# Kernel tuning notes

Hardware: AMD Instinct MI355X
Metric: run time of the kernel (lower is better)

The kernel has to match this reference:

```python
import jax, jax.numpy as jnp
import numpy as np

NUM_HEADS = 12

def _get_rel_pos(size, rel_pos):
    # q_size == k_size == size, no interpolation needed (table has 2*size-1 rows)
    idx = jnp.arange(size)[:, None] - jnp.arange(size)[None, :] + (size - 1)  # (size,size)
    return rel_pos[idx]  # (size, size, head_dim)

def setup_inputs() -> dict:
    key = jax.random.key(0)
    ks = jax.random.split(key, 7)
    B, H, W, dim = 8, 32, 32, 768
    head_dim = dim // NUM_HEADS
    return {
        "x": jax.random.normal(ks[0], (B, H, W, dim), jnp.float32),
        "qkv_w": jax.random.normal(ks[1], (dim, 3 * dim), jnp.float32) * 0.02,
        "qkv_b": jax.random.normal(ks[2], (3 * dim,), jnp.float32) * 0.02,
        "proj_w": jax.random.normal(ks[3], (dim, dim), jnp.float32) * 0.02,
        "proj_b": jax.random.normal(ks[4], (dim,), jnp.float32) * 0.02,
        "rel_pos_h": jax.random.normal(ks[5], (2 * H - 1, head_dim), jnp.float32) * 0.02,
        "rel_pos_w": jax.random.normal(ks[6], (2 * W - 1, head_dim), jnp.float32) * 0.02,
    }

def reference(x, qkv_w, qkv_b, proj_w, proj_b, rel_pos_h, rel_pos_w):
    B, H, W, dim = x.shape
    N = H * W
    head_dim = dim // NUM_HEADS
    scale = head_dim ** (-0.5)

    qkv = x.reshape(B, N, dim) @ qkv_w + qkv_b                     # (B,N,3*dim)
    qkv = qkv.reshape(B, N, 3, NUM_HEADS, head_dim)
    qkv = qkv.transpose(2, 0, 3, 1, 4).reshape(3, B * NUM_HEADS, N, head_dim)
    q, k, v = qkv[0], qkv[1], qkv[2]                               # (B*h, N, hd)

    attn = jnp.einsum("bnd,bmd->bnm", q * scale, k)                # (B*h, N, N)

    # decomposed relative position bias
    Rh = _get_rel_pos(H, rel_pos_h)                                # (H,H,hd)
    Rw = _get_rel_pos(W, rel_pos_w)                                # (W,W,hd)
    r_q = q.reshape(B * NUM_HEADS, H, W, head_dim)
    rel_h = jnp.einsum("bhwc,hkc->bhwk", r_q, Rh)                  # (B*h,H,W,H)
    rel_w = jnp.einsum("bhwc,wkc->bhwk", r_q, Rw)                  # (B*h,H,W,W)
    attn = (attn.reshape(B * NUM_HEADS, H, W, H, W)
            + rel_h[:, :, :, :, None]
            + rel_w[:, :, :, None, :]).reshape(B * NUM_HEADS, N, N)

    attn = jax.nn.softmax(attn, axis=-1)
    out = jnp.einsum("bnm,bmd->bnd", attn, v)                      # (B*h, N, hd)
    out = out.reshape(B, NUM_HEADS, H, W, head_dim).transpose(0, 2, 3, 1, 4).reshape(B, H, W, dim)
    return out @ proj_w + proj_b
```

## Files before the change

kernel.cpp:

```cpp
#include <hip/hip_runtime.h>
#include <hip/hip_bf16.h>
#include <math.h>

#define DIM   768
#define NHEAD 12
#define NQ    1024

typedef short  short8  __attribute__((ext_vector_type(8)));
typedef unsigned short us8 __attribute__((ext_vector_type(8)));
typedef float  f32x16  __attribute__((ext_vector_type(16)));

#if __has_builtin(__builtin_amdgcn_exp2f)
#define EXP2(x) __builtin_amdgcn_exp2f(x)
#else
#define EXP2(x) __expf(0.69314718056f * (x))
#endif
#define LOG2E 1.44269504089f

__device__ inline ushort f2b(float f) {
  union { float f; unsigned u; } c; c.f = f;
  unsigned r = (c.u + 0x7FFFu + ((c.u >> 16) & 1u)) >> 16;
  return (ushort)r;
}
__device__ inline float b2f(ushort h) {
  union { unsigned u; float f; } c; c.u = ((unsigned)h) << 16;
  return c.f;
}
__device__ inline ushort4 cvt4(float4 v) {
  ushort4 o; o.x = f2b(v.x); o.y = f2b(v.y); o.z = f2b(v.z); o.w = f2b(v.w);
  return o;
}
__device__ inline unsigned pkr(float a, float b) {
  union { float f; unsigned u; } ca, cb; ca.f = a; cb.f = b;
  return __builtin_amdgcn_perm(cb.u + 0x8000u, ca.u + 0x8000u, 0x07060302u);
}

__global__ __launch_bounds__(256) void prep(
    const float* __restrict__ x, const float* __restrict__ qkv_w,
    const float* __restrict__ proj_w, ushort* __restrict__ Xb,
    ushort* __restrict__ Wqt, ushort* __restrict__ Wpt) {
  __shared__ ushort Ts[64][68];
  const int blk = blockIdx.x, tid = threadIdx.x;
  if (blk < 768) {
    const float4* src = (const float4*)x;
    ushort4* dst = (ushort4*)Xb;
    int base = blk * 2048;
#pragma unroll
    for (int it = 0; it < 8; ++it) {
      int i = base + it * 256 + tid;
      dst[i] = cvt4(src[i]);
    }
    return;
  }
  const float* W; ushort* Wt; int ncols, tk, tn;
  if (blk < 1200) { int t = blk - 768;  W = qkv_w; Wt = Wqt; ncols = 2304; tk = t % 12; tn = t / 12; }
  else            { int t = blk - 1200; W = proj_w; Wt = Wpt; ncols = 768; tk = t % 12; tn = t / 12; }
  const int kb = tk * 64, nb = tn * 64;
#pragma unroll
  for (int rr = 0; rr < 4; ++rr) {
    int r = (tid >> 4) + rr * 16, c4 = (tid & 15) * 4;
    float4 w = *(const float4*)(W + (size_t)(kb + r) * ncols + nb + c4);
    *(ushort4*)&Ts[r][c4] = cvt4(w);
  }
  __syncthreads();
#pragma unroll
  for (int wwi = 0; wwi < 2; ++wwi) {
    int n = (tid >> 3) + wwi * 32, k8 = (tid & 7) * 8;
    us8 v;
#pragma unroll
    for (int j = 0; j < 8; ++j) v[j] = Ts[k8 + j][n];
    *(us8*)(Wt + (size_t)(nb + n) * 768 + kb + k8) = v;
  }
}

template <int OUTBF>
__global__ __launch_bounds__(256, 3) void gemm_mfma(
    const ushort* __restrict__ A, const ushort* __restrict__ BT,
    const float* __restrict__ bias, void* __restrict__ Cp, int Nc,
    ushort* __restrict__ VTg) {
  __shared__ ushort Asl[128][72];
  __shared__ ushort Bsl[128][72];
  const int tid = threadIdx.x;
  const int bm = blockIdx.y * 128, bn = blockIdx.x * 128;
  const int lane = tid & 63, wv = tid >> 6;
  const int l31 = lane & 31, lh = lane >> 5;
  const int wm = (wv >> 1) * 64, wn = (wv & 1) * 64;

  f32x16 acc[2][2];
#pragma unroll
  for (int i = 0; i < 2; ++i)
#pragma unroll
    for (int j = 0; j < 2; ++j)
#pragma unroll
      for (int r = 0; r < 16; ++r) acc[i][j][r] = 0.f;

  for (int kt = 0; kt < 768; kt += 64) {
    __syncthreads();
#pragma unroll
    for (int it = 0; it < 4; ++it) {
      int item = tid + 256 * it;
      int r = item >> 3, c8 = (item & 7) * 8;
      *(us8*)&Asl[r][c8] = *(const us8*)(A + (size_t)(bm + r) * 768 + kt + c8);
      *(us8*)&Bsl[r][c8] = *(const us8*)(BT + (size_t)(bn + r) * 768 + kt + c8);
    }
    __syncthreads();
#pragma unroll
    for (int ks = 0; ks < 4; ++ks) {
      short8 a0 = *(const short8*)&Asl[wm + l31][ks * 16 + lh * 8];
      short8 a1 = *(const short8*)&Asl[wm + 32 + l31][ks * 16 + lh * 8];
      short8 b0 = *(const short8*)&Bsl[wn + l31][ks * 16 + lh * 8];
      short8 b1 = *(const short8*)&Bsl[wn + 32 + l31][ks * 16 + lh * 8];
      acc[0][0] = __builtin_amdgcn_mfma_f32_32x32x16_bf16(a0, b0, acc[0][0], 0, 0, 0);
      acc[0][1] = __builtin_amdgcn_mfma_f32_32x32x16_bf16(a0, b1, acc[0][1], 0, 0, 0);
      acc[1][0] = __builtin_amdgcn_mfma_f32_32x32x16_bf16(a1, b0, acc[1][0], 0, 0, 0);
      acc[1][1] = __builtin_amdgcn_mfma_f32_32x32x16_bf16(a1, b1, acc[1][1], 0, 0, 0);
    }
  }

  const bool vreg = OUTBF && (bn >= 1536);
  if (!vreg) {
#pragma unroll
    for (int mb = 0; mb < 2; ++mb)
#pragma unroll
      for (int nb = 0; nb < 2; ++nb) {
        int col = bn + wn + nb * 32 + l31;
        float bv = bias[col];
#pragma unroll
        for (int reg = 0; reg < 16; ++reg) {
          int row = bm + wm + mb * 32 + (reg & 3) + 8 * (reg >> 2) + 4 * lh;
          float o = acc[mb][nb][reg] + bv;
          if (OUTBF) ((ushort*)Cp)[(size_t)row * Nc + col] = f2b(o);
          else       ((float*)Cp)[(size_t)row * Nc + col] = o;
        }
      }
  } else {
    const int b_ = bm >> 10;
    const int nbase = (bm & 1023) + wm;
#pragma unroll
    for (int nb = 0; nb < 2; ++nb) {
      int col = bn + wn + nb * 32 + l31;
      float bv = bias[col];
      int hd_ = col - 1536;
      int h_ = hd_ >> 6, d_ = hd_ & 63;
      ushort* vrow = VTg + ((size_t)(b_ * NHEAD + h_) * 64 + d_) * NQ;
#pragma unroll
      for (int mb = 0; mb < 2; ++mb)
#pragma unroll
        for (int g = 0; g < 4; ++g) {
          int n = nbase + mb * 32 + 8 * g + 4 * lh;
          ushort4 st;
          st.x = f2b(acc[mb][nb][4 * g + 0] + bv);
          st.y = f2b(acc[mb][nb][4 * g + 1] + bv);
          st.z = f2b(acc[mb][nb][4 * g + 2] + bv);
          st.w = f2b(acc[mb][nb][4 * g + 3] + bv);
          *(ushort4*)(vrow + n) = st;
        }
    }
  }
}

__global__ __launch_bounds__(256) void bias_kernel(
    const ushort* __restrict__ QKV, const float* __restrict__ rph,
    const float* __restrict__ rpw, ushort* __restrict__ RH,
    ushort* __restrict__ RW) {
  __shared__ ushort Qb[128][72];
  __shared__ ushort Tb[63][72];

  const int tid = threadIdx.x;
  const int bh = blockIdx.x;
  const int gy = blockIdx.y;
  const int b = bh / NHEAD, h = bh % NHEAD;
  const bool isH = gy < 8;
  const int g4 = isH ? gy : (gy - 8);
  const int lane = tid & 63, wv = tid >> 6;
  const int l31 = lane & 31, lh = lane >> 5;

  const ushort* qb = QKV + (size_t)b * NQ * 2304 + h * 64;
  const float* tab = isH ? rph : rpw;

#pragma unroll
  for (int it = 0; it < 4; ++it) {
    int item = tid + 256 * it;
    if (item < 63 * 16) {
      int r = item >> 4, q4 = (item & 15) * 4;
      float4 v = *(const float4*)(tab + r * 64 + q4);
      *(ushort4*)&Tb[r][q4] = cvt4(v);
    }
  }
#pragma unroll
  for (int it = 0; it < 4; ++it) {
    int item = tid + 256 * it;
    int r = item >> 3, c8 = (item & 7) * 8;
    int n = isH ? (g4 * 128 + r) : ((r & 31) * 32 + g4 * 4 + (r >> 5));
    *(us8*)&Qb[r][c8] = *(const us8*)(qb + (size_t)n * 2304 + c8);
  }
  __syncthreads();

  const int fixed = g4 * 4 + wv;
  f32x16 acc;
#pragma unroll
  for (int i = 0; i < 16; ++i) acc[i] = 0.f;
#pragma unroll
  for (int ks = 0; ks < 4; ++ks) {
    short8 a  = *(const short8*)&Qb[wv * 32 + l31][ks * 16 + lh * 8];
    short8 bb = *(const short8*)&Tb[fixed + 31 - l31][ks * 16 + lh * 8];
    acc = __builtin_amdgcn_mfma_f32_32x32x16_bf16(a, bb, acc, 0, 0, 0);
  }
  ushort* outp = isH ? RH : RW;
#pragma unroll
  for (int reg = 0; reg < 16; ++reg) {
    int row = (reg & 3) + 8 * (reg >> 2) + 4 * lh;
    int n = isH ? (fixed * 32 + row) : (row * 32 + fixed);
    outp[((size_t)bh * NQ + n) * 32 + l31] = f2b(acc[reg] * LOG2E);
  }
}

__global__ __launch_bounds__(256, 3) void attn_mfma(
    const ushort* __restrict__ QKV, const ushort* __restrict__ VTg,
    const ushort* __restrict__ RH, const ushort* __restrict__ RW,
    ushort* __restrict__ O) {
  __shared__ ushort Qs[128][72];
  __shared__ ushort Ks[64][72];
  __shared__ ushort VT[64][72];

  const int tid = threadIdx.x;
  const int bh = blockIdx.x % 96;
  const int qt = blockIdx.x / 96;
  const int b = bh / NHEAD, h = bh % NHEAD;
  const int n0 = qt * 128;
  const int lane = tid & 63, wv = tid >> 6;
  const int l31 = lane & 31, lh = lane >> 5;
  const int wb = wv * 32;

  const ushort* qb = QKV + (size_t)b * NQ * 2304 + h * 64;
  const ushort* kb = qb + DIM;
  const ushort* vtg = VTg + (size_t)bh * 64 * NQ;

#pragma unroll
  for (int it = 0; it < 4; ++it) {
    int item = tid + 256 * it;
    int r = item >> 3, c8 = (item & 7) * 8;
    *(us8*)&Qs[r][c8] = *(const us8*)(qb + (size_t)(n0 + r) * 2304 + c8);
  }

  const int q = n0 + wb + l31;
  const ushort* rwrow = RW + ((size_t)bh * NQ + q) * 32;
  float rwv[16];
#pragma unroll
  for (int g = 0; g < 4; ++g) {
    ushort4 v = *(const ushort4*)(rwrow + 8 * g + 4 * lh);
    rwv[4 * g + 0] = b2f(v.x); rwv[4 * g + 1] = b2f(v.y);
    rwv[4 * g + 2] = b2f(v.z); rwv[4 * g + 3] = b2f(v.w);
  }
  const ushort* rhrow = RH + ((size_t)bh * NQ + q) * 32;

  __syncthreads();
  short8 aq[4];
#pragma unroll
  for (int ks = 0; ks < 4; ++ks)
    aq[ks] = *(const short8*)&Qs[wb + l31][ks * 16 + lh * 8];

  ushort* Pb2 = &Qs[0][0] + wv * (32 * 40);

  f32x16 oacc0, oacc1;
#pragma unroll
  for (int i = 0; i < 16; ++i) { oacc0[i] = 0.f; oacc1[i] = 0.f; }
  float lacc = 0.f;

  for (int t = 0; t < 16; ++t) {
    const int kt = t * 64;
    __syncthreads();
    const unsigned rhu = *(const unsigned*)(rhrow + 2 * t);
#pragma unroll
    for (int it = 0; it < 2; ++it) {
      int item = tid + 256 * it;
      int r = item >> 3, c8 = (item & 7) * 8;
      *(us8*)&Ks[r][c8] = *(const us8*)(kb + (size_t)(kt + r) * 2304 + c8);
    }
#pragma unroll
    for (int it = 0; it < 2; ++it) {
      int item = tid + 256 * it;
      int d = item >> 3, j8 = (item & 7) * 8;
      *(us8*)&VT[d][j8] = *(const us8*)(vtg + (size_t)d * NQ + kt + j8);
    }
    __syncthreads();

    const float rh0 = b2f((ushort)(rhu & 0xFFFF));
    const float rh1 = b2f((ushort)(rhu >> 16));

#pragma unroll
    for (int cb = 0; cb < 2; ++cb) {
      f32x16 s;
#pragma unroll
      for (int i = 0; i < 16; ++i) s[i] = 0.f;
#pragma unroll
      for (int ks = 0; ks < 4; ++ks) {
        short8 ak = *(const short8*)&Ks[cb * 32 + l31][ks * 16 + lh * 8];
        s = __builtin_amdgcn_mfma_f32_32x32x16_bf16(ak, aq[ks], s, 0, 0, 0);
      }
      const float rhv = cb ? rh1 : rh0;
#pragma unroll
      for (int g = 0; g < 4; ++g) {
        float p0 = EXP2(fmaf(s[4 * g + 0], 0.18033688f, rwv[4 * g + 0] + rhv));
        float p1 = EXP2(fmaf(s[4 * g + 1], 0.18033688f, rwv[4 * g + 1] + rhv));
        float p2 = EXP2(fmaf(s[4 * g + 2], 0.18033688f, rwv[4 * g + 2] + rhv));
        float p3 = EXP2(fmaf(s[4 * g + 3], 0.18033688f, rwv[4 * g + 3] + rhv));
        lacc += (p0 + p1) + (p2 + p3);
        uint2 pk; pk.x = pkr(p0, p1); pk.y = pkr(p2, p3);
        *(uint2*)&Pb2[l31 * 40 + 8 * g + 4 * lh] = pk;
      }
#pragma unroll
      for (int ks = 0; ks < 2; ++ks) {
        short8 ap  = *(const short8*)&Pb2[l31 * 40 + ks * 16 + lh * 8];
        short8 bv0 = *(const short8*)&VT[l31][cb * 32 + ks * 16 + lh * 8];
        short8 bv1 = *(const short8*)&VT[32 + l31][cb * 32 + ks * 16 + lh * 8];
        oacc0 = __builtin_amdgcn_mfma_f32_32x32x16_bf16(ap, bv0, oacc0, 0, 0, 0);
        oacc1 = __builtin_amdgcn_mfma_f32_32x32x16_bf16(ap, bv1, oacc1, 0, 0, 0);
      }
    }
  }

  lacc += __shfl_xor(lacc, 32);
  const float linv = 1.0f / lacc;
  ushort* ob = O + ((size_t)b * NQ + n0 + wb) * DIM + h * 64;
#pragma unroll
  for (int reg = 0; reg < 16; ++reg) {
    int row = (reg & 3) + 8 * (reg >> 2) + 4 * lh;
    float lq = __shfl(linv, row);
    ob[(size_t)row * DIM + l31]      = f2b(oacc0[reg] * lq);
    ob[(size_t)row * DIM + 32 + l31] = f2b(oacc1[reg] * lq);
  }
}

extern "C" void kernel_launch(void* const* d_in, const int* in_sizes, int n_in,
                              void* d_out, int out_size, void* d_ws, size_t ws_size,
                              hipStream_t stream) {
  const float* x      = (const float*)d_in[0];
  const float* qkv_w  = (const float*)d_in[1];
  const float* qkv_b  = (const float*)d_in[2];
  const float* proj_w = (const float*)d_in[3];
  const float* proj_b = (const float*)d_in[4];
  const float* rel_h  = (const float*)d_in[5];
  const float* rel_w  = (const float*)d_in[6];
  float* out = (float*)d_out;

  ushort* qkvb = (ushort*)d_ws;
  ushort* obuf = qkvb + (size_t)8192 * 2304;
  ushort* RH   = obuf + (size_t)8192 * DIM;
  ushort* RW   = RH + (size_t)96 * NQ * 32;
  ushort* Xb   = RW + (size_t)96 * NQ * 32;
  ushort* Wqt  = Xb + (size_t)8192 * DIM;
  ushort* Wpt  = Wqt + (size_t)2304 * DIM;
  ushort* VTg  = Wpt + (size_t)DIM * DIM;

  prep<<<dim3(1344), 256, 0, stream>>>(x, qkv_w, proj_w, Xb, Wqt, Wpt);

  gemm_mfma<1><<<dim3(2304 / 128, 8192 / 128), 256, 0, stream>>>(
      Xb, Wqt, qkv_b, qkvb, 2304, VTg);

  bias_kernel<<<dim3(96, 16), 256, 0, stream>>>(qkvb, rel_h, rel_w, RH, RW);

  attn_mfma<<<dim3(96 * 8), 256, 0, stream>>>(qkvb, VTg, RH, RW, obuf);

  gemm_mfma<0><<<dim3(768 / 128, 8192 / 128), 256, 0, stream>>>(
      obuf, Wpt, proj_b, out, 768, nullptr);
}
```

Baseline: 216.3 us.

## Load GEMM and attention tiles via global_load_lds into XOR-swizzled shared memory

Replaces the register-staged global-to-LDS copies in the GEMM and attention kernels with direct global_load_lds 16-byte transfers. The shared tiles become unpadded 64-column arrays with an XOR column swizzle, so reads avoid bank conflicts without padding. The GEMM occupancy hint rises from 3 to 4 blocks per CU. The aim is to cut VGPR pressure and instruction overhead on tile loads, at the risk of correctness issues with the swizzle and LDS-DMA addressing.

```diff
diff --git a/kernel.cpp b/kernel.cpp
--- a/kernel.cpp
+++ b/kernel.cpp
@@ -33,6 +33,11 @@
 __device__ inline unsigned pkr(float a, float b) {
   union { float f; unsigned u; } ca, cb; ca.f = a; cb.f = b;
   return __builtin_amdgcn_perm(cb.u + 0x8000u, ca.u + 0x8000u, 0x07060302u);
+}
+__device__ __forceinline__ void gload16(const void* g, void* l) {
+  __builtin_amdgcn_global_load_lds(
+      (const __attribute__((address_space(1))) void*)g,
+      (__attribute__((address_space(3))) void*)l, 16, 0, 0);
 }
 
 __global__ __launch_bounds__(256) void prep(
@@ -74,17 +79,25 @@
 }
 
 template <int OUTBF>
-__global__ __launch_bounds__(256, 3) void gemm_mfma(
+__global__ __launch_bounds__(256, 4) void gemm_mfma(
     const ushort* __restrict__ A, const ushort* __restrict__ BT,
     const float* __restrict__ bias, void* __restrict__ Cp, int Nc,
     ushort* __restrict__ VTg) {
-  __shared__ ushort Asl[128][72];
-  __shared__ ushort Bsl[128][72];
+  __shared__ __align__(16) ushort As[128 * 64];
+  __shared__ __align__(16) ushort Bs[128 * 64];
   const int tid = threadIdx.x;
   const int bm = blockIdx.y * 128, bn = blockIdx.x * 128;
   const int lane = tid & 63, wv = tid >> 6;
   const int l31 = lane & 31, lh = lane >> 5;
   const int wm = (wv >> 1) * 64, wn = (wv & 1) * 64;
+  const int xr = l31 & 7;
+
+  const int dr = lane >> 3;
+  const int ccol = ((lane & 7) ^ dr) * 8;
+  const ushort* ag = A + (size_t)(bm + wv * 32 + dr) * 768 + ccol;
+  const ushort* bg = BT + (size_t)(bn + wv * 32 + dr) * 768 + ccol;
+  ushort* al = &As[wv * 32 * 64];
+  ushort* bl = &Bs[wv * 32 * 64];
 
   f32x16 acc[2][2];
 #pragma unroll
@@ -97,19 +110,18 @@
   for (int kt = 0; kt < 768; kt += 64) {
     __syncthreads();
 #pragma unroll
-    for (int it = 0; it < 4; ++it) {
-      int item = tid + 256 * it;
-      int r = item >> 3, c8 = (item & 7) * 8;
-      *(us8*)&Asl[r][c8] = *(const us8*)(A + (size_t)(bm + r) * 768 + kt + c8);
-      *(us8*)&Bsl[r][c8] = *(const us8*)(BT + (size_t)(bn + r) * 768 + kt + c8);
+    for (int wi = 0; wi < 4; ++wi) {
+      gload16(ag + kt + wi * (8 * 768), al + wi * 512);
+      gload16(bg + kt + wi * (8 * 768), bl + wi * 512);
     }
     __syncthreads();
 #pragma unroll
     for (int ks = 0; ks < 4; ++ks) {
-      short8 a0 = *(const short8*)&Asl[wm + l31][ks * 16 + lh * 8];
-      short8 a1 = *(const short8*)&Asl[wm + 32 + l31][ks * 16 + lh * 8];
-      short8 b0 = *(const short8*)&Bsl[wn + l31][ks * 16 + lh * 8];
-      short8 b1 = *(const short8*)&Bsl[wn + 32 + l31][ks * 16 + lh * 8];
+      const int ca = ((ks * 2 + lh) ^ xr) * 8;
+      short8 a0 = *(const short8*)&As[(wm + l31) * 64 + ca];
+      short8 a1 = *(const short8*)&As[(wm + 32 + l31) * 64 + ca];
+      short8 b0 = *(const short8*)&Bs[(wn + l31) * 64 + ca];
+      short8 b1 = *(const short8*)&Bs[(wn + 32 + l31) * 64 + ca];
       acc[0][0] = __builtin_amdgcn_mfma_f32_32x32x16_bf16(a0, b0, acc[0][0], 0, 0, 0);
       acc[0][1] = __builtin_amdgcn_mfma_f32_32x32x16_bf16(a0, b1, acc[0][1], 0, 0, 0);
       acc[1][0] = __builtin_amdgcn_mfma_f32_32x32x16_bf16(a1, b0, acc[1][0], 0, 0, 0);
@@ -220,8 +232,8 @@
     const ushort* __restrict__ RH, const ushort* __restrict__ RW,
     ushort* __restrict__ O) {
   __shared__ ushort Qs[128][72];
-  __shared__ ushort Ks[64][72];
-  __shared__ ushort VT[64][72];
+  __shared__ __align__(16) ushort Ks[64 * 64];
+  __shared__ __align__(16) ushort VT[64 * 64];
 
   const int tid = threadIdx.x;
   const int bh = blockIdx.x % 96;
@@ -231,6 +243,7 @@
   const int lane = tid & 63, wv = tid >> 6;
   const int l31 = lane & 31, lh = lane >> 5;
   const int wb = wv * 32;
+  const int xr = l31 & 7;
 
   const ushort* qb = QKV + (size_t)b * NQ * 2304 + h * 64;
   const ushort* kb = qb + DIM;
@@ -254,6 +267,13 @@
   }
   const ushort* rhrow = RH + ((size_t)bh * NQ + q) * 32;
 
+  const int dr = lane >> 3;
+  const int ccol = ((lane & 7) ^ dr) * 8;
+  const ushort* kg = kb + (size_t)(wv * 16 + dr) * 2304 + ccol;
+  const ushort* vg = vtg + (size_t)(wv * 16 + dr) * NQ + ccol;
+  ushort* kl = &Ks[wv * 16 * 64];
+  ushort* vl = &VT[wv * 16 * 64];
+
   __syncthreads();
   short8 aq[4];
 #pragma unroll
@@ -271,18 +291,10 @@
     const int kt = t * 64;
     __syncthreads();
     const unsigned rhu = *(const unsigned*)(rhrow + 2 * t);
-#pragma unroll
-    for (int it = 0; it < 2; ++it) {
-      int item = tid + 256 * it;
-      int r = item >> 3, c8 = (item & 7) * 8;
-      *(us8*)&Ks[r][c8] = *(const us8*)(kb + (size_t)(kt + r) * 2304 + c8);
-    }
-#pragma unroll
-    for (int it = 0; it < 2; ++it) {
-      int item = tid + 256 * it;
-      int d = item >> 3, j8 = (item & 7) * 8;
-      *(us8*)&VT[d][j8] = *(const us8*)(vtg + (size_t)d * NQ + kt + j8);
-    }
+    gload16(kg + (size_t)kt * 2304,              kl);
+    gload16(kg + (size_t)kt * 2304 + 8 * 2304,   kl + 512);
+    gload16(vg + kt,                             vl);
+    gload16(vg + kt + 8 * NQ,                    vl + 512);
     __syncthreads();
 
     const float rh0 = b2f((ushort)(rhu & 0xFFFF));
@@ -295,7 +307,8 @@
       for (int i = 0; i < 16; ++i) s[i] = 0.f;
 #pragma unroll
       for (int ks = 0; ks < 4; ++ks) {
-        short8 ak = *(const short8*)&Ks[cb * 32 + l31][ks * 16 + lh * 8];
+        const int ck = ((ks * 2 + lh) ^ xr) * 8;
+        short8 ak = *(const short8*)&Ks[(cb * 32 + l31) * 64 + ck];
         s = __builtin_amdgcn_mfma_f32_32x32x16_bf16(ak, aq[ks], s, 0, 0, 0);
       }
       const float rhv = cb ? rh1 : rh0;
@@ -311,9 +324,10 @@
       }
 #pragma unroll
       for (int ks = 0; ks < 2; ++ks) {
+        const int cv = ((cb * 4 + ks * 2 + lh) ^ xr) * 8;
         short8 ap  = *(const short8*)&Pb2[l31 * 40 + ks * 16 + lh * 8];
-        short8 bv0 = *(const short8*)&VT[l31][cb * 32 + ks * 16 + lh * 8];
-        short8 bv1 = *(const short8*)&VT[32 + l31][cb * 32 + ks * 16 + lh * 8];
+        short8 bv0 = *(const short8*)&VT[l31 * 64 + cv];
+        short8 bv1 = *(const short8*)&VT[(32 + l31) * 64 + cv];
         oacc0 = __builtin_amdgcn_mfma_f32_32x32x16_bf16(ap, bv0, oacc0, 0, 0, 0);
         oacc1 = __builtin_amdgcn_mfma_f32_32x32x16_bf16(ap, bv1, oacc1, 0, 0, 0);
       }
```

Result: faster. 207.6 us (-4.0%).
